# Kernel tuning notes

Measured on AMD Instinct MI355X. Metric: run time of the kernel, lower is better.

The kernel has to match this reference:

```python
import jax, jax.numpy as jnp
import numpy as np

F = 32          # features
L2 = 16         # (max_degree+1)^2 spherical components, max_degree=3
K = 16          # num radial basis functions
CUTOFF = 6.0
GAMMA = 1.0
NZ = 119        # max_atomic_number + 1
KE = 14.399645  # Coulomb constant, eV*Angstrom
ZBL_C = np.array([0.18175, 0.50986, 0.28022, 0.02817], dtype=np.float32)
ZBL_D = np.array([3.19980, 0.94229, 0.40290, 0.20162], dtype=np.float32)


def _smooth_cutoff(r):
    u = jnp.minimum(r / CUTOFF, 1.0 - 1e-6)
    return jnp.where(r < CUTOFF, jnp.exp(-u * u / (1.0 - u * u)), 0.0)


def _radial(r):
    # exponential-Chebyshev radial basis: T_k(2*exp(-gamma*r)-1), k=0..K-1
    t = jnp.clip(2.0 * jnp.exp(-GAMMA * r) - 1.0, -1.0, 1.0)
    ks = jnp.arange(K, dtype=jnp.float32)
    return jnp.cos(ks[None, :] * jnp.arccos(t)[:, None])  # (E,K)


def _sph_harm(u):
    # real spherical harmonics up to l=3 on unit vectors u (E,3) -> (E,16)
    x, y, z = u[:, 0], u[:, 1], u[:, 2]
    x2, y2, z2 = x * x, y * y, z * z
    return jnp.stack([
        jnp.full_like(x, 0.282095),
        0.488603 * y, 0.488603 * z, 0.488603 * x,
        1.092548 * x * y, 1.092548 * y * z, 0.315392 * (3.0 * z2 - 1.0),
        1.092548 * x * z, 0.546274 * (x2 - y2),
        0.590044 * y * (3.0 * x2 - y2), 2.890611 * x * y * z,
        0.457046 * y * (5.0 * z2 - 1.0), 0.373176 * z * (5.0 * z2 - 3.0),
        0.457046 * x * (5.0 * z2 - 1.0), 1.445306 * z * (x2 - y2),
        0.590044 * x * (x2 - 3.0 * y2),
    ], axis=-1)


def setup_inputs() -> dict:
    key = jax.random.key(0)
    ks = jax.random.split(key, 16)
    N, E, B = 16384, 262144, 512
    atomic_numbers = jax.random.randint(ks[0], (N,), 0, 18)
    positions = jax.random.normal(ks[1], (N, 3), dtype=jnp.float32) * 3.0
    dst_idx = jax.random.randint(ks[2], (E,), 0, N)
    src_idx = jax.random.randint(ks[3], (E,), 0, N)
    batch_segments = jnp.sort(jax.random.randint(ks[4], (N,), 0, B))
    p = lambda k, shp, s: jax.random.normal(k, shp, dtype=jnp.float32) * s
    return {
        "atomic_numbers": atomic_numbers,
        "positions": positions,
        "dst_idx": dst_idx,
        "src_idx": src_idx,
        "batch_segments": batch_segments,
        "batch_size": B,
        "batch_mask": jnp.ones((B,), dtype=jnp.float32),
        "atom_mask": jnp.ones((N,), dtype=jnp.float32),
        "embed": p(ks[5], (NZ, F), 0.1),
        "Wr1_0": p(ks[6], (K, F), 0.25),
        "Wr2_0": p(ks[7], (K, F), 0.25),
        "W1_0": p(ks[8], (F, F), 0.18),
        "W2_0": p(ks[9], (F, F), 0.18),
        "Wr1_1": p(ks[10], (K, F), 0.25),
        "W1_1": p(ks[11], (F, F), 0.18),
        "W2_1": p(ks[12], (F, F), 0.18),
        "w_out": p(ks[13], (F,), 0.1),
        "b_out": p(ks[14], (NZ,), 0.1),
    }


def reference(atomic_numbers, positions, dst_idx, src_idx, batch_segments,
              batch_size, batch_mask, atom_mask, embed,
              Wr1_0, Wr2_0, W1_0, W2_0, Wr1_1, W1_1, W2_1, w_out, b_out):
    N = positions.shape[0]
    # ---- geometric features (gather on edges) ----
    disp = positions[src_idx] - positions[dst_idx]          # (E,3)
    r = jnp.sqrt(jnp.sum(disp * disp, axis=-1) + 1e-10)     # (E,)
    r = jnp.maximum(r, 1e-4)
    cut = _smooth_cutoff(r)                                  # (E,)
    rad = _radial(r) * cut[:, None]                          # (E,K)
    sh = _sph_harm(disp / r[:, None])                        # (E,L2)

    # ---- atom embedding lifted to equivariant features (N,L2,F) ----
    x = jnp.zeros((N, L2, F), dtype=jnp.float32).at[:, 0, :].set(embed[atomic_numbers])

    # ---- iteration 0: full-degree message passing ----
    g1 = rad @ Wr1_0                                         # (E,F) scalar->tensor path
    g2 = rad @ Wr2_0                                         # (E,F) degree-preserving path
    xs = x[src_idx]                                          # (E,L2,F)
    m = sh[:, :, None] * (g1[:, None, :] * xs[:, 0:1, :]) + g2[:, None, :] * xs
    x = jax.ops.segment_sum(m, dst_idx, num_segments=N)      # (N,L2,F)
    # refinement (equivariant gated residual MLP)
    h = jnp.einsum('nlf,fg->nlg', x, W1_0)
    x = x + jnp.einsum('nlf,fg->nlg', h * jax.nn.silu(h[:, 0:1, :]), W2_0)

    # ---- iteration 1: max_degree=0 message passing ----
    x0 = x[:, 0, :]                                          # (N,F)
    g = rad @ Wr1_1                                          # (E,F)
    x0 = jax.ops.segment_sum(g * x0[src_idx], dst_idx, num_segments=N)
    x0 = x0 + jax.nn.silu(x0 @ W1_1) @ W2_1                  # scalar refinement

    # ---- atomic energy readout ----
    e_atom = x0 @ w_out + b_out[atomic_numbers]              # (N,)

    # ---- ZBL nuclear repulsion over edges ----
    zf = atomic_numbers.astype(jnp.float32)
    zd, zs = zf[dst_idx], zf[src_idx]
    a = 0.8854 * 0.529177 / (zd ** 0.23 + zs ** 0.23 + 1e-10)
    phi = jnp.sum(ZBL_C[None, :] * jnp.exp(-ZBL_D[None, :] * (r / a)[:, None]), axis=-1)
    e_pair = 0.5 * KE * zd * zs / r * phi * cut
    e_atom = e_atom + jax.ops.segment_sum(e_pair, dst_idx, num_segments=N)

    e_atom = e_atom * atom_mask
    # scatter atomic energies to molecules
    e_mol = jax.ops.segment_sum(e_atom, batch_segments, num_segments=batch_size)
    return e_mol * batch_mask                                # (B,)
```

## Files before the change

### kernel.cpp

```cpp
#include <hip/hip_runtime.h>
#include <hip/hip_fp16.h>


#define FDIM 32
#define KDIM 16
#define BINCAP 32
#define MAXZ 18

__device__ __forceinline__ int pack_ct(float cut, float tt) {
    unsigned lo = __half_as_ushort(__float2half_rn(cut));
    unsigned hi = __half_as_ushort(__float2half_rn(tt));
    return (int)((hi << 16) | lo);
}
__device__ __forceinline__ float unpack_cut(int w) {
    return __half2float(__ushort_as_half((unsigned short)(w & 0xFFFF)));
}
__device__ __forceinline__ float unpack_tt(int w) {
    return __half2float(__ushort_as_half((unsigned short)(((unsigned)w) >> 16)));
}

__global__ __launch_bounds__(256) void zero_k(int* __restrict__ p, int n2,
                                              float* __restrict__ o, int b) {
    int i = blockIdx.x * 256 + threadIdx.x;
    if (i < n2) p[i] = 0;
    if (i < b) o[i] = 0.f;
}

__global__ __launch_bounds__(256) void edge_k(
    const int* __restrict__ dst, const int* __restrict__ src,
    const int* __restrict__ Z, const float* __restrict__ pos,
    int* __restrict__ counts, float* __restrict__ pair,
    int2* __restrict__ bins, int E)
{
    __shared__ float zpow[MAXZ];
    int tid = threadIdx.x;
    if (tid < MAXZ) zpow[tid] = __powf((float)tid, 0.23f);
    __syncthreads();

    int i = blockIdx.x * 256 + tid;
    if (i >= E) return;
    int d = dst[i], s = src[i];
    float ax = pos[3 * s], ay = pos[3 * s + 1], az = pos[3 * s + 2];
    float bx = pos[3 * d], by = pos[3 * d + 1], bz = pos[3 * d + 2];
    float dx = ax - bx, dy = ay - by, dz = az - bz;
    float r2 = dx * dx + dy * dy + dz * dz;
    if (r2 >= 36.0f) return;

    int zs_i = Z[s], zd_i = Z[d];
    float r = fmaxf(sqrtf(r2 + 1e-10f), 1e-4f);
    float u = r * (1.0f / 6.0f);
    float u2 = u * u;
    float cut = __expf(-u2 / (1.0f - u2));
    float tt = fminf(fmaxf(2.0f * __expf(-r) - 1.0f, -1.0f), 1.0f);
    float zd = (float)zd_i, zsf = (float)zs_i;
    float zsum = zpow[zd_i] + zpow[zs_i] + 1e-10f;
    float ra = r * zsum * (1.0f / 0.46853312f);
    float phi = 0.18175f * __expf(-3.1998f  * ra)
              + 0.50986f * __expf(-0.94229f * ra)
              + 0.28022f * __expf(-0.4029f  * ra)
              + 0.02817f * __expf(-0.20162f * ra);
    atomicAdd(&pair[d], 0.5f * 14.399645f * zd * zsf / r * phi * cut);
    int slot = atomicAdd(&counts[d], 1);
    if (slot < BINCAP)
        bins[d * BINCAP + slot] = make_int2(s | (zs_i << 14), pack_ct(cut, tt));
}

__global__ __launch_bounds__(256) void gather1_k(
    const int* __restrict__ counts, const int2* __restrict__ bins,
    const float* __restrict__ embed, const float* __restrict__ Wr1_0,
    const float* __restrict__ Wr2_0, const float* __restrict__ W1_0,
    const float* __restrict__ W2_0, float* __restrict__ x0, int N)
{
    __shared__ float Wc[KDIM * FDIM];
    __shared__ float W1s[FDIM * FDIM];
    __shared__ float W2s[FDIM * FDIM];
    __shared__ float emb_s[MAXZ * FDIM];
    int tid = threadIdx.x;
    for (int i = tid; i < KDIM * FDIM; i += 256)
        Wc[i] = 0.282095f * Wr1_0[i] + Wr2_0[i];
    for (int i = tid; i < FDIM * FDIM; i += 256) { W1s[i] = W1_0[i]; W2s[i] = W2_0[i]; }
    for (int i = tid; i < MAXZ * FDIM; i += 256) emb_s[i] = embed[i];
    __syncthreads();

    int w = (blockIdx.x * 256 + tid) >> 6;
    int lane = tid & 63, f = lane & 31;
    int a = 2 * w + (lane >> 5);
    if (a >= N) return;
    int deg = min(counts[a], BINCAP);
    int dm = max(__shfl(deg, 0), __shfl(deg, 32));
    const int4* rq = (const int4*)(bins + (size_t)a * BINCAP);
    float acc = 0.f;
    for (int i = 0; i < dm; i += 4) {
        int4 ra = rq[i >> 1];
        int4 rb = rq[(i >> 1) + 1];
        bool v0 = i < deg, v1 = i + 1 < deg, v2 = i + 2 < deg, v3 = i + 3 < deg;
        float c0 = v0 ? unpack_cut(ra.y) : 0.f;
        float c1 = v1 ? unpack_cut(ra.w) : 0.f;
        float c2 = v2 ? unpack_cut(rb.y) : 0.f;
        float c3 = v3 ? unpack_cut(rb.w) : 0.f;
        int z0 = (ra.x >> 14) & 31, z1 = (ra.z >> 14) & 31;
        int z2 = (rb.x >> 14) & 31, z3 = (rb.z >> 14) & 31;
        float e0 = emb_s[(v0 ? z0 : 0) * FDIM + f];
        float e1 = emb_s[(v1 ? z1 : 0) * FDIM + f];
        float e2 = emb_s[(v2 ? z2 : 0) * FDIM + f];
        float e3 = emb_s[(v3 ? z3 : 0) * FDIM + f];
        float t0 = unpack_tt(ra.y), t1 = unpack_tt(ra.w);
        float t2 = unpack_tt(rb.y), t3 = unpack_tt(rb.w);
        float A0 = 1.f, A1 = t0, B0 = 1.f, B1 = t1;
        float C0 = 1.f, C1 = t2, D0 = 1.f, D1 = t3;
        float g0 = Wc[f] + Wc[FDIM + f] * t0;
        float g1 = Wc[f] + Wc[FDIM + f] * t1;
        float g2 = Wc[f] + Wc[FDIM + f] * t2;
        float g3 = Wc[f] + Wc[FDIM + f] * t3;
        #pragma unroll
        for (int k = 2; k < KDIM; ++k) {
            float A2 = 2.f * t0 * A1 - A0;
            float B2 = 2.f * t1 * B1 - B0;
            float C2 = 2.f * t2 * C1 - C0;
            float D2 = 2.f * t3 * D1 - D0;
            float wk = Wc[k * FDIM + f];
            g0 = fmaf(wk, A2, g0); g1 = fmaf(wk, B2, g1);
            g2 = fmaf(wk, C2, g2); g3 = fmaf(wk, D2, g3);
            A0 = A1; A1 = A2; B0 = B1; B1 = B2;
            C0 = C1; C1 = C2; D0 = D1; D1 = D2;
        }
        acc = fmaf(c0 * g0, e0, acc);
        acc = fmaf(c1 * g1, e1, acc);
        acc = fmaf(c2 * g2, e2, acc);
        acc = fmaf(c3 * g3, e3, acc);
    }
    float h = 0.f;
    #pragma unroll
    for (int g = 0; g < FDIM; ++g)
        h = fmaf(__shfl(acc, g, 32), W1s[g * FDIM + f], h);
    float cc = h * h / (1.0f + __expf(-h));
    float xo = acc;
    #pragma unroll
    for (int g = 0; g < FDIM; ++g)
        xo = fmaf(__shfl(cc, g, 32), W2s[g * FDIM + f], xo);
    x0[(size_t)a * FDIM + f] = xo;
}

__global__ __launch_bounds__(256) void gather2_k(
    const int* __restrict__ counts, const int2* __restrict__ bins,
    const float* __restrict__ x0, const float* __restrict__ pair,
    const float* __restrict__ Wr1_1, const float* __restrict__ W1_1,
    const float* __restrict__ W2_1, const float* __restrict__ w_out,
    const float* __restrict__ b_out, const int* __restrict__ Z,
    const int* __restrict__ bseg, const float* __restrict__ bmask,
    const float* __restrict__ amask, float* __restrict__ out, int N)
{
    __shared__ float Wg[KDIM * FDIM];
    __shared__ float W1s[FDIM * FDIM];
    __shared__ float W2s[FDIM * FDIM];
    __shared__ float wo[FDIM];
    int tid = threadIdx.x;
    for (int i = tid; i < KDIM * FDIM; i += 256) Wg[i] = Wr1_1[i];
    for (int i = tid; i < FDIM * FDIM; i += 256) { W1s[i] = W1_1[i]; W2s[i] = W2_1[i]; }
    if (tid < FDIM) wo[tid] = w_out[tid];
    __syncthreads();

    int w = (blockIdx.x * 256 + tid) >> 6;
    int lane = tid & 63, f = lane & 31;
    int a = 2 * w + (lane >> 5);
    if (a >= N) return;
    int deg = min(counts[a], BINCAP);
    int dm = max(__shfl(deg, 0), __shfl(deg, 32));
    const int4* rq = (const int4*)(bins + (size_t)a * BINCAP);
    float acc = 0.f;
    for (int i = 0; i < dm; i += 4) {
        int4 ra = rq[i >> 1];
        int4 rb = rq[(i >> 1) + 1];
        bool v0 = i < deg, v1 = i + 1 < deg, v2 = i + 2 < deg, v3 = i + 3 < deg;
        int s0 = v0 ? (ra.x & 0x3FFF) : 0;
        int s1 = v1 ? (ra.z & 0x3FFF) : 0;
        int s2 = v2 ? (rb.x & 0x3FFF) : 0;
        int s3 = v3 ? (rb.z & 0x3FFF) : 0;
        float xa = x0[(size_t)s0 * FDIM + f];
        float xb = x0[(size_t)s1 * FDIM + f];
        float xc = x0[(size_t)s2 * FDIM + f];
        float xd = x0[(size_t)s3 * FDIM + f];
        float c0 = v0 ? unpack_cut(ra.y) : 0.f;
        float c1 = v1 ? unpack_cut(ra.w) : 0.f;
        float c2 = v2 ? unpack_cut(rb.y) : 0.f;
        float c3 = v3 ? unpack_cut(rb.w) : 0.f;
        float t0 = unpack_tt(ra.y), t1 = unpack_tt(ra.w);
        float t2 = unpack_tt(rb.y), t3 = unpack_tt(rb.w);
        float A0 = 1.f, A1 = t0, B0 = 1.f, B1 = t1;
        float C0 = 1.f, C1 = t2, D0 = 1.f, D1 = t3;
        float g0 = Wg[f] + Wg[FDIM + f] * t0;
        float g1 = Wg[f] + Wg[FDIM + f] * t1;
        float g2 = Wg[f] + Wg[FDIM + f] * t2;
        float g3 = Wg[f] + Wg[FDIM + f] * t3;
        #pragma unroll
        for (int k = 2; k < KDIM; ++k) {
            float A2 = 2.f * t0 * A1 - A0;
            float B2 = 2.f * t1 * B1 - B0;
            float C2 = 2.f * t2 * C1 - C0;
            float D2 = 2.f * t3 * D1 - D0;
            float wk = Wg[k * FDIM + f];
            g0 = fmaf(wk, A2, g0); g1 = fmaf(wk, B2, g1);
            g2 = fmaf(wk, C2, g2); g3 = fmaf(wk, D2, g3);
            A0 = A1; A1 = A2; B0 = B1; B1 = B2;
            C0 = C1; C1 = C2; D0 = D1; D1 = D2;
        }
        acc = fmaf(c0 * g0, xa, acc);
        acc = fmaf(c1 * g1, xb, acc);
        acc = fmaf(c2 * g2, xc, acc);
        acc = fmaf(c3 * g3, xd, acc);
    }
    float h = 0.f;
    #pragma unroll
    for (int g = 0; g < FDIM; ++g)
        h = fmaf(__shfl(acc, g, 32), W1s[g * FDIM + f], h);
    float cc = h / (1.0f + __expf(-h));
    float xo = acc;
    #pragma unroll
    for (int g = 0; g < FDIM; ++g)
        xo = fmaf(__shfl(cc, g, 32), W2s[g * FDIM + f], xo);
    float ea = xo * wo[f];
    #pragma unroll
    for (int m = 16; m >= 1; m >>= 1) ea += __shfl_xor(ea, m, 32);
    if ((lane & 31) == 0) {
        float e_atom = ea + b_out[Z[a]] + pair[a];
        int b = bseg[a];
        atomicAdd(&out[b], e_atom * amask[a] * bmask[b]);
    }
}

extern "C" void kernel_launch(void* const* d_in, const int* in_sizes, int n_in,
                              void* d_out, int out_size, void* d_ws, size_t ws_size,
                              hipStream_t stream) {
    int N = in_sizes[0];
    int E = in_sizes[2];
    int B = in_sizes[6];

    const int*   Z      = (const int*)d_in[0];
    const float* pos    = (const float*)d_in[1];
    const int*   dst    = (const int*)d_in[2];
    const int*   src    = (const int*)d_in[3];
    const int*   bseg   = (const int*)d_in[4];
    const float* bmask  = (const float*)d_in[6];
    const float* amask  = (const float*)d_in[7];
    const float* embed  = (const float*)d_in[8];
    const float* Wr1_0  = (const float*)d_in[9];
    const float* Wr2_0  = (const float*)d_in[10];
    const float* W1_0   = (const float*)d_in[11];
    const float* W2_0   = (const float*)d_in[12];
    const float* Wr1_1  = (const float*)d_in[13];
    const float* W1_1   = (const float*)d_in[14];
    const float* W2_1   = (const float*)d_in[15];
    const float* w_out  = (const float*)d_in[16];
    const float* b_out  = (const float*)d_in[17];
    float* out = (float*)d_out;

    int2*  bins   = (int2*)d_ws;
    int*   counts = (int*)(bins + (size_t)N * BINCAP);
    float* pair   = (float*)(counts + N);
    float* x0     = pair + N;

    int zb = (2 * N + 255) / 256;
    zero_k<<<zb, 256, 0, stream>>>(counts, 2 * N, out, B);

    int eb = (E + 255) / 256;
    edge_k<<<eb, 256, 0, stream>>>(dst, src, Z, pos, counts, pair, bins, E);

    int gb = (N / 2 * 64 + 255) / 256;
    gather1_k<<<gb, 256, 0, stream>>>(counts, bins, embed, Wr1_0, Wr2_0,
                                      W1_0, W2_0, x0, N);
    gather2_k<<<gb, 256, 0, stream>>>(counts, bins, x0, pair, Wr1_1, W1_1, W2_1,
                                      w_out, b_out, Z, bseg, bmask, amask, out, N);
}
```

Before: 146.8 us.

## Fuse all stages into one persistent cooperative kernel with grid syncs

Replaces the four separate launches (zero, edge binning, two gather passes) with one cooperative persistent kernel that uses grid-wide syncs between phases and grid-stride loops. It is meant to remove per-launch overhead and the gaps between small kernels. The old multi-kernel path stays as a fallback if the cooperative launch fails. In exchange it pays for grid barriers, loads every stage's weights into shared memory (higher LDS use may lower occupancy), and runs with a capped grid instead of one thread per work item.

Measured after the change: 274.8 us. 1.87x slower.

```diff
diff --git a/kernel.cpp b/kernel.cpp
--- a/kernel.cpp
+++ b/kernel.cpp
@@ -1,11 +1,15 @@
 #include <hip/hip_runtime.h>
 #include <hip/hip_fp16.h>
+#include <hip/hip_cooperative_groups.h>
+
+namespace cg = cooperative_groups;
 
 
 #define FDIM 32
 #define KDIM 16
 #define BINCAP 32
 #define MAXZ 18
+#define BLK 256
 
 __device__ __forceinline__ int pack_ct(float cut, float tt) {
     unsigned lo = __half_as_ushort(__float2half_rn(cut));
@@ -17,6 +21,206 @@
 }
 __device__ __forceinline__ float unpack_tt(int w) {
     return __half2float(__ushort_as_half((unsigned short)(((unsigned)w) >> 16)));
+}
+
+__global__ __launch_bounds__(BLK) void fused_k(
+    const int* __restrict__ dst, const int* __restrict__ src,
+    const int* __restrict__ Z, const float* __restrict__ pos,
+    const int* __restrict__ bseg, const float* __restrict__ bmask,
+    const float* __restrict__ amask, const float* __restrict__ embed,
+    const float* __restrict__ Wr1_0, const float* __restrict__ Wr2_0,
+    const float* __restrict__ W1_0, const float* __restrict__ W2_0,
+    const float* __restrict__ Wr1_1, const float* __restrict__ W1_1,
+    const float* __restrict__ W2_1, const float* __restrict__ w_out,
+    const float* __restrict__ b_out, float* __restrict__ out,
+    int2* __restrict__ bins, int* __restrict__ counts,
+    float* __restrict__ pair, float* __restrict__ x0,
+    int N, int E, int B)
+{
+    cg::grid_group grid = cg::this_grid();
+
+    __shared__ float Wc[KDIM * FDIM];
+    __shared__ float Wg[KDIM * FDIM];
+    __shared__ float W1a[FDIM * FDIM], W2a[FDIM * FDIM];
+    __shared__ float W1b[FDIM * FDIM], W2b[FDIM * FDIM];
+    __shared__ float emb_s[MAXZ * FDIM];
+    __shared__ float wo[FDIM];
+    __shared__ float zpow[32];
+
+    int tid = threadIdx.x;
+    int gsize = gridDim.x * BLK;
+    int gtid = blockIdx.x * BLK + tid;
+
+    for (int i = tid; i < KDIM * FDIM; i += BLK) {
+        Wc[i] = 0.282095f * Wr1_0[i] + Wr2_0[i];
+        Wg[i] = Wr1_1[i];
+    }
+    for (int i = tid; i < FDIM * FDIM; i += BLK) {
+        W1a[i] = W1_0[i]; W2a[i] = W2_0[i];
+        W1b[i] = W1_1[i]; W2b[i] = W2_1[i];
+    }
+    for (int i = tid; i < MAXZ * FDIM; i += BLK) emb_s[i] = embed[i];
+    if (tid < FDIM) wo[tid] = w_out[tid];
+    if (tid < 32) zpow[tid] = __powf((float)tid, 0.23f);
+
+    for (int i = gtid; i < 2 * N; i += gsize) counts[i] = 0;
+    for (int i = gtid; i < B; i += gsize) out[i] = 0.f;
+    grid.sync();
+
+    for (int i = gtid; i < E; i += gsize) {
+        int d = dst[i], s = src[i];
+        float ax = pos[3 * s], ay = pos[3 * s + 1], az = pos[3 * s + 2];
+        float bx = pos[3 * d], by = pos[3 * d + 1], bz = pos[3 * d + 2];
+        float dx = ax - bx, dy = ay - by, dz = az - bz;
+        float r2 = dx * dx + dy * dy + dz * dz;
+        if (r2 >= 36.0f) continue;
+        int zs_i = Z[s], zd_i = Z[d];
+        float r = fmaxf(sqrtf(r2 + 1e-10f), 1e-4f);
+        float u = r * (1.0f / 6.0f);
+        float u2 = u * u;
+        float cut = __expf(-u2 / (1.0f - u2));
+        float tt = fminf(fmaxf(2.0f * __expf(-r) - 1.0f, -1.0f), 1.0f);
+        float zd = (float)zd_i, zsf = (float)zs_i;
+        float zsum = zpow[zd_i] + zpow[zs_i] + 1e-10f;
+        float ra = r * zsum * (1.0f / 0.46853312f);
+        float phi = 0.18175f * __expf(-3.1998f  * ra)
+                  + 0.50986f * __expf(-0.94229f * ra)
+                  + 0.28022f * __expf(-0.4029f  * ra)
+                  + 0.02817f * __expf(-0.20162f * ra);
+        atomicAdd(&pair[d], 0.5f * 14.399645f * zd * zsf / r * phi * cut);
+        int slot = atomicAdd(&counts[d], 1);
+        if (slot < BINCAP)
+            bins[d * BINCAP + slot] =
+                make_int2(s | (zs_i << 14), pack_ct(cut, tt));
+    }
+    grid.sync();
+
+    int nwave = gsize >> 6;
+    int gw = gtid >> 6;
+    int lane = tid & 63, f = lane & 31, half = lane >> 5;
+    for (int p = gw; p < N / 2; p += nwave) {
+        int a = 2 * p + half;
+        int deg = min(counts[a], BINCAP);
+        int dm = max(__shfl(deg, 0), __shfl(deg, 32));
+        const int4* rq = (const int4*)(bins + (size_t)a * BINCAP);
+        float acc = 0.f;
+        for (int i = 0; i < dm; i += 4) {
+            int4 ra = rq[i >> 1];
+            int4 rb = rq[(i >> 1) + 1];
+            bool v0 = i < deg, v1 = i + 1 < deg, v2 = i + 2 < deg, v3 = i + 3 < deg;
+            float c0 = v0 ? unpack_cut(ra.y) : 0.f;
+            float c1 = v1 ? unpack_cut(ra.w) : 0.f;
+            float c2 = v2 ? unpack_cut(rb.y) : 0.f;
+            float c3 = v3 ? unpack_cut(rb.w) : 0.f;
+            int z0 = (ra.x >> 14) & 31, z1 = (ra.z >> 14) & 31;
+            int z2 = (rb.x >> 14) & 31, z3 = (rb.z >> 14) & 31;
+            float e0 = emb_s[(v0 ? z0 : 0) * FDIM + f];
+            float e1 = emb_s[(v1 ? z1 : 0) * FDIM + f];
+            float e2 = emb_s[(v2 ? z2 : 0) * FDIM + f];
+            float e3 = emb_s[(v3 ? z3 : 0) * FDIM + f];
+            float t0 = unpack_tt(ra.y), t1 = unpack_tt(ra.w);
+            float t2 = unpack_tt(rb.y), t3 = unpack_tt(rb.w);
+            float A0 = 1.f, A1 = t0, B0 = 1.f, B1 = t1;
+            float C0 = 1.f, C1 = t2, D0 = 1.f, D1 = t3;
+            float g0 = Wc[f] + Wc[FDIM + f] * t0;
+            float g1 = Wc[f] + Wc[FDIM + f] * t1;
+            float g2 = Wc[f] + Wc[FDIM + f] * t2;
+            float g3 = Wc[f] + Wc[FDIM + f] * t3;
+            #pragma unroll
+            for (int k = 2; k < KDIM; ++k) {
+                float A2 = 2.f * t0 * A1 - A0;
+                float B2 = 2.f * t1 * B1 - B0;
+                float C2 = 2.f * t2 * C1 - C0;
+                float D2 = 2.f * t3 * D1 - D0;
+                float wk = Wc[k * FDIM + f];
+                g0 = fmaf(wk, A2, g0); g1 = fmaf(wk, B2, g1);
+                g2 = fmaf(wk, C2, g2); g3 = fmaf(wk, D2, g3);
+                A0 = A1; A1 = A2; B0 = B1; B1 = B2;
+                C0 = C1; C1 = C2; D0 = D1; D1 = D2;
+            }
+            acc = fmaf(c0 * g0, e0, acc);
+            acc = fmaf(c1 * g1, e1, acc);
+            acc = fmaf(c2 * g2, e2, acc);
+            acc = fmaf(c3 * g3, e3, acc);
+        }
+        float h = 0.f;
+        #pragma unroll
+        for (int g = 0; g < FDIM; ++g)
+            h = fmaf(__shfl(acc, g, 32), W1a[g * FDIM + f], h);
+        float cc = h * h / (1.0f + __expf(-h));
+        float xo = acc;
+        #pragma unroll
+        for (int g = 0; g < FDIM; ++g)
+            xo = fmaf(__shfl(cc, g, 32), W2a[g * FDIM + f], xo);
+        x0[(size_t)a * FDIM + f] = xo;
+    }
+    grid.sync();
+
+    for (int p = gw; p < N / 2; p += nwave) {
+        int a = 2 * p + half;
+        int deg = min(counts[a], BINCAP);
+        int dm = max(__shfl(deg, 0), __shfl(deg, 32));
+        const int4* rq = (const int4*)(bins + (size_t)a * BINCAP);
+        float acc = 0.f;
+        for (int i = 0; i < dm; i += 4) {
+            int4 ra = rq[i >> 1];
+            int4 rb = rq[(i >> 1) + 1];
+            bool v0 = i < deg, v1 = i + 1 < deg, v2 = i + 2 < deg, v3 = i + 3 < deg;
+            int s0 = v0 ? (ra.x & 0x3FFF) : 0;
+            int s1 = v1 ? (ra.z & 0x3FFF) : 0;
+            int s2 = v2 ? (rb.x & 0x3FFF) : 0;
+            int s3 = v3 ? (rb.z & 0x3FFF) : 0;
+            float xa = x0[(size_t)s0 * FDIM + f];
+            float xb = x0[(size_t)s1 * FDIM + f];
+            float xc = x0[(size_t)s2 * FDIM + f];
+            float xd = x0[(size_t)s3 * FDIM + f];
+            float c0 = v0 ? unpack_cut(ra.y) : 0.f;
+            float c1 = v1 ? unpack_cut(ra.w) : 0.f;
+            float c2 = v2 ? unpack_cut(rb.y) : 0.f;
+            float c3 = v3 ? unpack_cut(rb.w) : 0.f;
+            float t0 = unpack_tt(ra.y), t1 = unpack_tt(ra.w);
+            float t2 = unpack_tt(rb.y), t3 = unpack_tt(rb.w);
+            float A0 = 1.f, A1 = t0, B0 = 1.f, B1 = t1;
+            float C0 = 1.f, C1 = t2, D0 = 1.f, D1 = t3;
+            float g0 = Wg[f] + Wg[FDIM + f] * t0;
+            float g1 = Wg[f] + Wg[FDIM + f] * t1;
+            float g2 = Wg[f] + Wg[FDIM + f] * t2;
+            float g3 = Wg[f] + Wg[FDIM + f] * t3;
+            #pragma unroll
+            for (int k = 2; k < KDIM; ++k) {
+                float A2 = 2.f * t0 * A1 - A0;
+                float B2 = 2.f * t1 * B1 - B0;
+                float C2 = 2.f * t2 * C1 - C0;
+                float D2 = 2.f * t3 * D1 - D0;
+                float wk = Wg[k * FDIM + f];
+                g0 = fmaf(wk, A2, g0); g1 = fmaf(wk, B2, g1);
+                g2 = fmaf(wk, C2, g2); g3 = fmaf(wk, D2, g3);
+                A0 = A1; A1 = A2; B0 = B1; B1 = B2;
+                C0 = C1; C1 = C2; D0 = D1; D1 = D2;
+            }
+            acc = fmaf(c0 * g0, xa, acc);
+            acc = fmaf(c1 * g1, xb, acc);
+            acc = fmaf(c2 * g2, xc, acc);
+            acc = fmaf(c3 * g3, xd, acc);
+        }
+        float h = 0.f;
+        #pragma unroll
+        for (int g = 0; g < FDIM; ++g)
+            h = fmaf(__shfl(acc, g, 32), W1b[g * FDIM + f], h);
+        float cc = h / (1.0f + __expf(-h));
+        float xo = acc;
+        #pragma unroll
+        for (int g = 0; g < FDIM; ++g)
+            xo = fmaf(__shfl(cc, g, 32), W2b[g * FDIM + f], xo);
+        float ea = xo * wo[f];
+        #pragma unroll
+        for (int m = 16; m >= 1; m >>= 1) ea += __shfl_xor(ea, m, 32);
+        if ((lane & 31) == 0) {
+            float e_atom = ea + b_out[Z[a]] + pair[a];
+            int b = bseg[a];
+            atomicAdd(&out[b], e_atom * amask[a] * bmask[b]);
+        }
+    }
 }
 
 __global__ __launch_bounds__(256) void zero_k(int* __restrict__ p, int n2,
@@ -36,7 +240,6 @@
     int tid = threadIdx.x;
     if (tid < MAXZ) zpow[tid] = __powf((float)tid, 0.23f);
     __syncthreads();
-
     int i = blockIdx.x * 256 + tid;
     if (i >= E) return;
     int d = dst[i], s = src[i];
@@ -45,7 +248,6 @@
     float dx = ax - bx, dy = ay - by, dz = az - bz;
     float r2 = dx * dx + dy * dy + dz * dz;
     if (r2 >= 36.0f) return;
-
     int zs_i = Z[s], zd_i = Z[d];
     float r = fmaxf(sqrtf(r2 + 1e-10f), 1e-4f);
     float u = r * (1.0f / 6.0f);
@@ -81,7 +283,6 @@
     for (int i = tid; i < FDIM * FDIM; i += 256) { W1s[i] = W1_0[i]; W2s[i] = W2_0[i]; }
     for (int i = tid; i < MAXZ * FDIM; i += 256) emb_s[i] = embed[i];
     __syncthreads();
-
     int w = (blockIdx.x * 256 + tid) >> 6;
     int lane = tid & 63, f = lane & 31;
     int a = 2 * w + (lane >> 5);
@@ -159,7 +360,6 @@
     for (int i = tid; i < FDIM * FDIM; i += 256) { W1s[i] = W1_1[i]; W2s[i] = W2_1[i]; }
     if (tid < FDIM) wo[tid] = w_out[tid];
     __syncthreads();
-
     int w = (blockIdx.x * 256 + tid) >> 6;
     int lane = tid & 63, f = lane & 31;
     int a = 2 * w + (lane >> 5);
@@ -259,15 +459,39 @@
     float* pair   = (float*)(counts + N);
     float* x0     = pair + N;
 
-    int zb = (2 * N + 255) / 256;
-    zero_k<<<zb, 256, 0, stream>>>(counts, 2 * N, out, B);
-
-    int eb = (E + 255) / 256;
-    edge_k<<<eb, 256, 0, stream>>>(dst, src, Z, pos, counts, pair, bins, E);
-
-    int gb = (N / 2 * 64 + 255) / 256;
-    gather1_k<<<gb, 256, 0, stream>>>(counts, bins, embed, Wr1_0, Wr2_0,
-                                      W1_0, W2_0, x0, N);
-    gather2_k<<<gb, 256, 0, stream>>>(counts, bins, x0, pair, Wr1_1, W1_1, W2_1,
-                                      w_out, b_out, Z, bseg, bmask, amask, out, N);
-}
+    int blocksPerCU = 0;
+    hipError_t qerr = hipOccupancyMaxActiveBlocksPerMultiprocessor(
+        &blocksPerCU, fused_k, BLK, 0);
+    int grid = 0;
+    if (qerr == hipSuccess && blocksPerCU > 0) {
+        grid = blocksPerCU * 256;
+        if (grid > 2048) grid = 2048;
+    }
+
+    hipError_t lerr = hipErrorUnknown;
+    if (grid > 0) {
+        void* args[] = {
+            (void*)&dst, (void*)&src, (void*)&Z, (void*)&pos,
+            (void*)&bseg, (void*)&bmask, (void*)&amask, (void*)&embed,
+            (void*)&Wr1_0, (void*)&Wr2_0, (void*)&W1_0, (void*)&W2_0,
+            (void*)&Wr1_1, (void*)&W1_1, (void*)&W2_1, (void*)&w_out,
+            (void*)&b_out, (void*)&out, (void*)&bins, (void*)&counts,
+            (void*)&pair, (void*)&x0, (void*)&N, (void*)&E, (void*)&B
+        };
+        lerr = hipLaunchCooperativeKernel((const void*)fused_k, dim3(grid),
+                                          dim3(BLK), args, 0, stream);
+    }
+
+    if (lerr != hipSuccess) {
+        int zb = (2 * N + 255) / 256;
+        zero_k<<<zb, 256, 0, stream>>>(counts, 2 * N, out, B);
+        int eb = (E + 255) / 256;
+        edge_k<<<eb, 256, 0, stream>>>(dst, src, Z, pos, counts, pair, bins, E);
+        int gb = (N / 2 * 64 + 255) / 256;
+        gather1_k<<<gb, 256, 0, stream>>>(counts, bins, embed, Wr1_0, Wr2_0,
+                                          W1_0, W2_0, x0, N);
+        gather2_k<<<gb, 256, 0, stream>>>(counts, bins, x0, pair, Wr1_1, W1_1,
+                                          W2_1, w_out, b_out, Z, bseg, bmask,
+                                          amask, out, N);
+    }
+}
```
